# Kernel tuning notes

Measured on AMD Instinct MI355X. Metric: run time of the kernel, lower is better.

The kernel has to match this reference:

```python
import jax, jax.numpy as jnp
import numpy as np

N = 50000          # nodes
E = 800000         # edges (before self-loops)
F_IN = 128         # num_features
HEADS = 4
OUT = 128 // HEADS # per-head channels = num_hidden // heads
NEG_SLOPE = 0.2    # PyG GATConv default


def setup_inputs() -> dict:
    key = jax.random.key(0)
    ks = jax.random.split(key, 10)
    x = jax.random.normal(ks[0], (N, F_IN), jnp.float32)
    edge_index = jax.random.randint(ks[1], (2, E), 0, N, dtype=jnp.int64)
    sW = 1.0 / np.sqrt(F_IN)
    sA = 1.0 / np.sqrt(OUT)
    return {
        "x": x,
        "edge_index": edge_index,
        "W1": jax.random.normal(ks[2], (F_IN, HEADS * OUT), jnp.float32) * sW,
        "a_src1": jax.random.normal(ks[3], (HEADS, OUT), jnp.float32) * sA,
        "a_dst1": jax.random.normal(ks[4], (HEADS, OUT), jnp.float32) * sA,
        "b1": jnp.zeros((HEADS * OUT,), jnp.float32),
        "W2": jax.random.normal(ks[5], (HEADS * OUT, HEADS * OUT), jnp.float32) * sW,
        "a_src2": jax.random.normal(ks[6], (HEADS, OUT), jnp.float32) * sA,
        "a_dst2": jax.random.normal(ks[7], (HEADS, OUT), jnp.float32) * sA,
        "b2": jnp.zeros((HEADS * OUT,), jnp.float32),
    }


def gat_conv(x, src, dst, W, a_src, a_dst, b):
    """One GATConv layer (PyG semantics, concat heads, self-loops already in src/dst)."""
    n = x.shape[0]
    h = (x @ W).reshape(n, HEADS, OUT)                 # [N, H, C]
    # per-node attention halves, gathered per edge -> [Etot, H]
    alpha = (h * a_src).sum(-1)[src] + (h * a_dst).sum(-1)[dst]
    alpha = jax.nn.leaky_relu(alpha, NEG_SLOPE)
    # softmax over incoming edges of each destination node (stable)
    amax = jax.ops.segment_max(alpha, dst, num_segments=n)
    ex = jnp.exp(alpha - amax[dst])
    denom = jax.ops.segment_sum(ex, dst, num_segments=n)
    attn = ex / (denom[dst] + 1e-16)                    # [Etot, H]
    # weighted message scatter-add
    out = jax.ops.segment_sum(h[src] * attn[..., None], dst, num_segments=n)
    return out.reshape(n, HEADS * OUT) + b


def reference(x, edge_index, W1, a_src1, a_dst1, b1, W2, a_src2, a_dst2, b2):
    loops = jnp.arange(N, dtype=edge_index.dtype)       # PyG add_self_loops=True
    src = jnp.concatenate([edge_index[0], loops])
    dst = jnp.concatenate([edge_index[1], loops])
    h = jax.nn.relu(gat_conv(x, src, dst, W1, a_src1, a_dst1, b1))
    # dropout = identity in eval mode
    h = jax.nn.relu(gat_conv(h, src, dst, W2, a_src2, a_dst2, b2))
    return h
```

## Files before the change

### kernel.cpp

```cpp
#include <hip/hip_runtime.h>
#include <hip/hip_fp16.h>
#include <cstdint>
#include <cstddef>

#define NN 50000
#define EE 800000
#define ETOT (EE + NN)
#define FD 128
#define NH 4
#define NEG_SLOPE 0.2f

#define BSHIFT 10
#define BSIZE 1024
#define NBKT ((NN + BSIZE - 1) / BSIZE)
#define CAPG 20000
#define CHUNK 2048
#define P1_BLOCKS ((ETOT + CHUNK - 1) / CHUNK)

typedef _Float16 half8 __attribute__((ext_vector_type(8)));
typedef float f32x4 __attribute__((ext_vector_type(4)));


__global__ __launch_bounds__(256) void bin_kernel(const int* __restrict__ ei,
                                                  int* __restrict__ gcnt,
                                                  uint32_t* __restrict__ gbkt) {
    __shared__ int lcnt[NBKT];
    __shared__ int gb[NBKT];
    const int t = threadIdx.x;
    if (t < NBKT) lcnt[t] = 0;
    __syncthreads();
    const int base = blockIdx.x * CHUNK;
    uint32_t pk[8]; int bk[8]; int sl[8];
    #pragma unroll
    for (int j = 0; j < 8; ++j) {
        int e = base + j * 256 + t;
        bk[j] = -1;
        if (e < ETOT) {
            int src, dst;
            if (e < EE) { src = ei[e]; dst = ei[EE + e]; }
            else        { src = e - EE; dst = src; }
            int b = dst >> BSHIFT;
            bk[j] = b;
            pk[j] = (uint32_t)src | ((uint32_t)(dst & (BSIZE - 1)) << 16);
            sl[j] = atomicAdd(&lcnt[b], 1);
        }
    }
    __syncthreads();
    if (t < NBKT) gb[t] = atomicAdd(&gcnt[t], lcnt[t]);
    __syncthreads();
    #pragma unroll
    for (int j = 0; j < 8; ++j)
        if (bk[j] >= 0)
            gbkt[(size_t)bk[j] * CAPG + gb[bk[j]] + sl[j]] = pk[j];
}

__global__ void bktscan_kernel(const int* __restrict__ gcnt, int* __restrict__ bbase,
                               int* __restrict__ row_ptr) {
    int lane = threadIdx.x;
    int v = (lane < NBKT) ? gcnt[lane] : 0;
    int inc = v;
    #pragma unroll
    for (int off = 1; off < 64; off <<= 1) {
        int u = __shfl_up(inc, off);
        if (lane >= off) inc += u;
    }
    if (lane < NBKT) bbase[lane] = inc - v;
    if (lane == 0) row_ptr[NN] = ETOT;
}

__global__ __launch_bounds__(1024) void sort_kernel(const int* __restrict__ gcnt,
                                                    const int* __restrict__ bbase,
                                                    const uint32_t* __restrict__ gbkt,
                                                    int* __restrict__ row_ptr,
                                                    int* __restrict__ csr) {
    __shared__ int cnt[BSIZE];
    __shared__ int pfx[BSIZE];
    __shared__ int wsum[16];
    const int b = blockIdx.x;
    const int t = threadIdx.x;
    const int count = gcnt[b];
    const int cbase = bbase[b];
    const int dstBase = b << BSHIFT;
    const int ndst = (NN - dstBase < BSIZE) ? (NN - dstBase) : BSIZE;
    const uint32_t* mybkt = gbkt + (size_t)b * CAPG;
    cnt[t] = 0;
    __syncthreads();
    for (int i = t; i < count; i += 1024)
        atomicAdd(&cnt[mybkt[i] >> 16], 1);
    __syncthreads();
    int v = cnt[t];
    int inc = v;
    const int lane = t & 63, wid = t >> 6;
    #pragma unroll
    for (int off = 1; off < 64; off <<= 1) {
        int u = __shfl_up(inc, off);
        if (lane >= off) inc += u;
    }
    if (lane == 63) wsum[wid] = inc;
    __syncthreads();
    if (t < 16) {
        int w = wsum[t]; int wi = w;
        #pragma unroll
        for (int off = 1; off < 16; off <<= 1) {
            int u = __shfl_up(wi, off);
            if (t >= off) wi += u;
        }
        wsum[t] = wi - w;
    }
    __syncthreads();
    int excl = wsum[wid] + inc - v;
    pfx[t] = excl;
    if (t < ndst) row_ptr[dstBase + t] = cbase + excl;
    cnt[t] = 0;
    __syncthreads();
    for (int i = t; i < count; i += 1024) {
        uint32_t pkv = mybkt[i];
        int dl = pkv >> 16;
        int r = atomicAdd(&cnt[dl], 1);
        csr[cbase + pfx[dl] + r] = (int)(pkv & 0xFFFFu);
    }
}


__global__ void prep_kernel(const float* __restrict__ W1, const float* __restrict__ W2,
                            uint4* __restrict__ Wf1, uint4* __restrict__ Wf2) {
    const float* W = blockIdx.x ? W2 : W1;
    uint4* Wf = blockIdx.x ? Wf2 : Wf1;
    for (int s = threadIdx.x; s < 2048; s += 256) {
        int fi = s >> 6;
        int lane = s & 63;
        int ct = fi >> 2, ks = fi & 3;
        int col = ct * 16 + (lane & 15);
        int kb = ks * 32 + (lane >> 4) * 8;
        half8 h;
        #pragma unroll
        for (int j = 0; j < 8; ++j) h[j] = (_Float16)W[(kb + j) * FD + col];
        Wf[s] = *(uint4*)&h;
    }
}


__global__ __launch_bounds__(256) void gemm_kernel(const float* __restrict__ X,
                                                   const uint4* __restrict__ Wf,
                                                   __half* __restrict__ Hh) {
    const int tid = threadIdx.x;
    const int wv = tid >> 6, lane = tid & 63;
    const int l15 = lane & 15, lg = lane >> 4;
    const int rowA = blockIdx.x * 64 + wv * 16 + l15;
    const int rA = (rowA < NN) ? rowA : NN - 1;
    half8 a[4];
    #pragma unroll
    for (int ks = 0; ks < 4; ++ks) {
        int kb = ks * 32 + lg * 8;
        float4 x0 = *(const float4*)&X[(size_t)rA * FD + kb];
        float4 x1 = *(const float4*)&X[(size_t)rA * FD + kb + 4];
        a[ks][0] = (_Float16)x0.x; a[ks][1] = (_Float16)x0.y;
        a[ks][2] = (_Float16)x0.z; a[ks][3] = (_Float16)x0.w;
        a[ks][4] = (_Float16)x1.x; a[ks][5] = (_Float16)x1.y;
        a[ks][6] = (_Float16)x1.z; a[ks][7] = (_Float16)x1.w;
    }
    const int rowC = blockIdx.x * 64 + wv * 16 + lg * 4;
    #pragma unroll
    for (int ct = 0; ct < 8; ++ct) {
        uint4 braw[4];
        #pragma unroll
        for (int ks = 0; ks < 4; ++ks) braw[ks] = Wf[(ct * 4 + ks) * 64 + lane];
        f32x4 acc = {0.f, 0.f, 0.f, 0.f};
        #pragma unroll
        for (int ks = 0; ks < 4; ++ks) {
            half8 b = *(half8*)&braw[ks];
            acc = __builtin_amdgcn_mfma_f32_16x16x32_f16(a[ks], b, acc, 0, 0, 0);
        }
        #pragma unroll
        for (int r = 0; r < 4; ++r) {
            int gr = rowC + r;
            if (gr < NN) Hh[(size_t)gr * FD + ct * 16 + l15] = __float2half(acc[r]);
        }
    }
}


__global__ __launch_bounds__(256) void adot_kernel(const __half* __restrict__ H,
                                                   const float* __restrict__ a_src,
                                                   const float* __restrict__ a_dst,
                                                   float* __restrict__ AS,
                                                   float* __restrict__ AD) {
    int gt = blockIdx.x * 256 + threadIdx.x;
    int n = gt >> 4;
    int l = gt & 15;
    if (n >= NN) return;
    union { uint4 u; __half2 q[4]; } hv;
    hv.u = *(const uint4*)&H[(size_t)n * FD + l * 8];
    float ps = 0.f, pd = 0.f;
    #pragma unroll
    for (int j = 0; j < 4; ++j) {
        float2 f = __half22float2(hv.q[j]);
        ps += f.x * a_src[l * 8 + 2 * j] + f.y * a_src[l * 8 + 2 * j + 1];
        pd += f.x * a_dst[l * 8 + 2 * j] + f.y * a_dst[l * 8 + 2 * j + 1];
    }
    ps += __shfl_xor(ps, 1); ps += __shfl_xor(ps, 2);
    pd += __shfl_xor(pd, 1); pd += __shfl_xor(pd, 2);
    if ((l & 3) == 0) {
        AS[n * NH + (l >> 2)] = ps;
        AD[n * NH + (l >> 2)] = pd;
    }
}


__device__ __forceinline__ float sel4(float a0, float a1, float a2, float a3, int h) {
    float lo = (h & 1) ? a1 : a0;
    float hi = (h & 1) ? a3 : a2;
    return (h & 2) ? hi : lo;
}

__global__ __launch_bounds__(256) void agg_kernel(const __half* __restrict__ H,
                                                  const float* __restrict__ AS,
                                                  const float* __restrict__ AD,
                                                  const int* __restrict__ row_ptr,
                                                  const int* __restrict__ csr_src,
                                                  const float* __restrict__ bias,
                                                  float* __restrict__ Out) {
    __shared__ float sP[8][32][5];
    __shared__ int   sS[8][32];
    const int wave = threadIdx.x >> 6;
    const int lane = threadIdx.x & 63;
    const int sub  = lane >> 5;
    const int sl   = lane & 31;
    const int ws   = wave * 2 + sub;
    const int n = blockIdx.x * 8 + ws;
    const int start = row_ptr[n], end = row_ptr[n + 1];
    const int h0 = sl >> 3;
    const float4 adv = *(const float4*)&AD[n * NH];
    float s[NH] = {0.f, 0.f, 0.f, 0.f};
    float acc0 = 0.f, acc1 = 0.f, acc2 = 0.f, acc3 = 0.f;

    for (int base = start; base < end; base += 32) {
        int cn = end - base; if (cn > 32) cn = 32;
        int my_src = 0;
        float al[NH];
        if (sl < cn) {
            my_src = csr_src[base + sl];
            float4 asv = *(const float4*)&AS[my_src * NH];
            al[0] = asv.x + adv.x; al[1] = asv.y + adv.y;
            al[2] = asv.z + adv.z; al[3] = asv.w + adv.w;
        }
        sS[ws][sl] = my_src;
        #pragma unroll
        for (int h = 0; h < NH; ++h) {
            float a = al[h];
            a = (a > 0.f) ? a : NEG_SLOPE * a;
            float p = (sl < cn) ? __expf(a) : 0.f;
            sP[ws][sl][h] = p;
            #pragma unroll
            for (int off = 16; off; off >>= 1) p += __shfl_xor(p, off, 32);
            s[h] += p;
        }
        #pragma unroll 4
        for (int e = 0; e < cn; ++e) {
            float pm = sP[ws][e][h0];
            int se = sS[ws][e];
            union { uint2 u; __half2 q[2]; } hv;
            hv.u = *(const uint2*)&H[(size_t)se * FD + sl * 4];
            float2 f0 = __half22float2(hv.q[0]);
            float2 f1 = __half22float2(hv.q[1]);
            acc0 += pm * f0.x; acc1 += pm * f0.y;
            acc2 += pm * f1.x; acc3 += pm * f1.y;
        }
    }
    float sh = sel4(s[0], s[1], s[2], s[3], h0);
    float inv = 1.f / (sh + 1e-16f);
    const float4 bv = *(const float4*)&bias[sl * 4];
    float4 ov;
    ov.x = fmaxf(acc0 * inv + bv.x, 0.f);
    ov.y = fmaxf(acc1 * inv + bv.y, 0.f);
    ov.z = fmaxf(acc2 * inv + bv.z, 0.f);
    ov.w = fmaxf(acc3 * inv + bv.w, 0.f);
    *(float4*)&Out[(size_t)n * FD + sl * 4] = ov;
}


extern "C" void kernel_launch(void* const* d_in, const int* in_sizes, int n_in,
                              void* d_out, int out_size, void* d_ws, size_t ws_size,
                              hipStream_t stream) {
    const float* x     = (const float*)d_in[0];
    const int*   ei    = (const int*)d_in[1];
    const float* W1    = (const float*)d_in[2];
    const float* asrc1 = (const float*)d_in[3];
    const float* adst1 = (const float*)d_in[4];
    const float* b1    = (const float*)d_in[5];
    const float* W2    = (const float*)d_in[6];
    const float* asrc2 = (const float*)d_in[7];
    const float* adst2 = (const float*)d_in[8];
    const float* b2    = (const float*)d_in[9];
    float* out = (float*)d_out;

    char* p = (char*)d_ws;
    auto alloc = [&](size_t bytes) {
        char* q = p;
        p += (bytes + 255) & ~(size_t)255;
        return q;
    };
    int*      row_ptr = (int*)alloc((NN + 1) * sizeof(int));
    int*      gcnt    = (int*)alloc(NBKT * sizeof(int));
    int*      bbase   = (int*)alloc(NBKT * sizeof(int));
    uint32_t* gbkt    = (uint32_t*)alloc((size_t)NBKT * CAPG * sizeof(uint32_t));
    int*      csr     = (int*)alloc((size_t)ETOT * sizeof(int));
    float*    AS      = (float*)alloc((size_t)NN * NH * sizeof(float));
    float*    AD      = (float*)alloc((size_t)NN * NH * sizeof(float));
    __half*   Hh      = (__half*)alloc((size_t)NN * FD * sizeof(__half));
    uint4*    Wf1     = (uint4*)alloc(2048 * sizeof(uint4));
    uint4*    Wf2     = (uint4*)alloc(2048 * sizeof(uint4));
    (void)ws_size; (void)in_sizes; (void)n_in; (void)out_size;

    hipMemsetAsync(gcnt, 0, NBKT * sizeof(int), stream);
    bin_kernel<<<P1_BLOCKS, 256, 0, stream>>>(ei, gcnt, gbkt);
    prep_kernel<<<2, 256, 0, stream>>>(W1, W2, Wf1, Wf2);
    bktscan_kernel<<<1, 64, 0, stream>>>(gcnt, bbase, row_ptr);
    sort_kernel<<<NBKT, 1024, 0, stream>>>(gcnt, bbase, gbkt, row_ptr, csr);

    gemm_kernel<<<(NN + 63) / 64, 256, 0, stream>>>(x, Wf1, Hh);
    adot_kernel<<<(NN * 16 + 255) / 256, 256, 0, stream>>>(Hh, asrc1, adst1, AS, AD);
    agg_kernel<<<NN / 8, 256, 0, stream>>>(Hh, AS, AD, row_ptr, csr, b1, out);

    gemm_kernel<<<(NN + 63) / 64, 256, 0, stream>>>(out, Wf2, Hh);
    adot_kernel<<<(NN * 16 + 255) / 256, 256, 0, stream>>>(Hh, asrc2, adst2, AS, AD);
    agg_kernel<<<NN / 8, 256, 0, stream>>>(Hh, AS, AD, row_ptr, csr, b2, out);
}
```

Before: 157.4 us.

## Fuse attention dot products into GEMM epilogue and merge preprocessing launches

The per-node attention projections (AS/AD) are now computed inside the GEMM epilogue from the fp32 MFMA accumulators, using a butterfly shuffle transpose-reduce. This removes the separate adot kernel and its re-read of H. The weight-prep work is folded into extra blocks of the binning kernel, and the bucket scan is recomputed redundantly inside each sort block. The memset becomes a tiny kernel, so two fewer launches run per layer pipeline. In exchange the GEMM epilogue uses more registers and shuffles, and the attention logits now come from fp32 accumulators instead of fp16-rounded H, which slightly changes numerics.

After: 193.4 us. 1.23x slower.

```diff
diff --git a/kernel.cpp b/kernel.cpp
--- a/kernel.cpp
+++ b/kernel.cpp
@@ -21,9 +21,35 @@
 typedef float f32x4 __attribute__((ext_vector_type(4)));
 
 
+__global__ void zero_kernel(int* __restrict__ gcnt) {
+    int t = threadIdx.x;
+    if (t < NBKT) gcnt[t] = 0;
+}
+
+
 __global__ __launch_bounds__(256) void bin_kernel(const int* __restrict__ ei,
                                                   int* __restrict__ gcnt,
-                                                  uint32_t* __restrict__ gbkt) {
+                                                  uint32_t* __restrict__ gbkt,
+                                                  const float* __restrict__ W1,
+                                                  const float* __restrict__ W2,
+                                                  uint4* __restrict__ Wf1,
+                                                  uint4* __restrict__ Wf2) {
+    if (blockIdx.x >= P1_BLOCKS) {
+        const float* W = (blockIdx.x - P1_BLOCKS) ? W2 : W1;
+        uint4* Wf = (blockIdx.x - P1_BLOCKS) ? Wf2 : Wf1;
+        for (int s = threadIdx.x; s < 2048; s += 256) {
+            int fi = s >> 6;
+            int lane = s & 63;
+            int ct = fi >> 2, ks = fi & 3;
+            int col = ct * 16 + (lane & 15);
+            int kb = ks * 32 + (lane >> 4) * 8;
+            half8 h;
+            #pragma unroll
+            for (int j = 0; j < 8; ++j) h[j] = (_Float16)W[(kb + j) * FD + col];
+            Wf[s] = *(uint4*)&h;
+        }
+        return;
+    }
     __shared__ int lcnt[NBKT];
     __shared__ int gb[NBKT];
     const int t = threadIdx.x;
@@ -54,37 +80,34 @@
             gbkt[(size_t)bk[j] * CAPG + gb[bk[j]] + sl[j]] = pk[j];
 }
 
-__global__ void bktscan_kernel(const int* __restrict__ gcnt, int* __restrict__ bbase,
-                               int* __restrict__ row_ptr) {
-    int lane = threadIdx.x;
-    int v = (lane < NBKT) ? gcnt[lane] : 0;
-    int inc = v;
-    #pragma unroll
-    for (int off = 1; off < 64; off <<= 1) {
-        int u = __shfl_up(inc, off);
-        if (lane >= off) inc += u;
-    }
-    if (lane < NBKT) bbase[lane] = inc - v;
-    if (lane == 0) row_ptr[NN] = ETOT;
-}
 
 __global__ __launch_bounds__(1024) void sort_kernel(const int* __restrict__ gcnt,
-                                                    const int* __restrict__ bbase,
                                                     const uint32_t* __restrict__ gbkt,
                                                     int* __restrict__ row_ptr,
                                                     int* __restrict__ csr) {
     __shared__ int cnt[BSIZE];
     __shared__ int pfx[BSIZE];
     __shared__ int wsum[16];
+    __shared__ int sCbase;
     const int b = blockIdx.x;
     const int t = threadIdx.x;
     const int count = gcnt[b];
-    const int cbase = bbase[b];
     const int dstBase = b << BSHIFT;
     const int ndst = (NN - dstBase < BSIZE) ? (NN - dstBase) : BSIZE;
     const uint32_t* mybkt = gbkt + (size_t)b * CAPG;
     cnt[t] = 0;
-    __syncthreads();
+    if (t < 64) {
+        int v = (t < NBKT) ? gcnt[t] : 0;
+        int inc = v;
+        #pragma unroll
+        for (int off = 1; off < 64; off <<= 1) {
+            int u = __shfl_up(inc, off);
+            if (t >= off) inc += u;
+        }
+        if (t == b) sCbase = inc - v;
+    }
+    __syncthreads();
+    const int cbase = sCbase;
     for (int i = t; i < count; i += 1024)
         atomicAdd(&cnt[mybkt[i] >> 16], 1);
     __syncthreads();
@@ -111,6 +134,7 @@
     int excl = wsum[wid] + inc - v;
     pfx[t] = excl;
     if (t < ndst) row_ptr[dstBase + t] = cbase + excl;
+    if (b == NBKT - 1 && t == 0) row_ptr[NN] = ETOT;
     cnt[t] = 0;
     __syncthreads();
     for (int i = t; i < count; i += 1024) {
@@ -122,27 +146,13 @@
 }
 
 
-__global__ void prep_kernel(const float* __restrict__ W1, const float* __restrict__ W2,
-                            uint4* __restrict__ Wf1, uint4* __restrict__ Wf2) {
-    const float* W = blockIdx.x ? W2 : W1;
-    uint4* Wf = blockIdx.x ? Wf2 : Wf1;
-    for (int s = threadIdx.x; s < 2048; s += 256) {
-        int fi = s >> 6;
-        int lane = s & 63;
-        int ct = fi >> 2, ks = fi & 3;
-        int col = ct * 16 + (lane & 15);
-        int kb = ks * 32 + (lane >> 4) * 8;
-        half8 h;
-        #pragma unroll
-        for (int j = 0; j < 8; ++j) h[j] = (_Float16)W[(kb + j) * FD + col];
-        Wf[s] = *(uint4*)&h;
-    }
-}
-
-
 __global__ __launch_bounds__(256) void gemm_kernel(const float* __restrict__ X,
                                                    const uint4* __restrict__ Wf,
-                                                   __half* __restrict__ Hh) {
+                                                   const float* __restrict__ a_src,
+                                                   const float* __restrict__ a_dst,
+                                                   __half* __restrict__ Hh,
+                                                   float* __restrict__ AS,
+                                                   float* __restrict__ AD) {
     const int tid = threadIdx.x;
     const int wv = tid >> 6, lane = tid & 63;
     const int l15 = lane & 15, lg = lane >> 4;
@@ -159,7 +169,14 @@
         a[ks][4] = (_Float16)x1.x; a[ks][5] = (_Float16)x1.y;
         a[ks][6] = (_Float16)x1.z; a[ks][7] = (_Float16)x1.w;
     }
+    float asr[8], adr[8];
+    #pragma unroll
+    for (int ct = 0; ct < 8; ++ct) {
+        asr[ct] = a_src[ct * 16 + l15];
+        adr[ct] = a_dst[ct * 16 + l15];
+    }
     const int rowC = blockIdx.x * 64 + wv * 16 + lg * 4;
+    float ps[NH][4] = {}, pd[NH][4] = {};
     #pragma unroll
     for (int ct = 0; ct < 8; ++ct) {
         uint4 braw[4];
@@ -168,8 +185,13 @@
         f32x4 acc = {0.f, 0.f, 0.f, 0.f};
         #pragma unroll
         for (int ks = 0; ks < 4; ++ks) {
-            half8 b = *(half8*)&braw[ks];
-            acc = __builtin_amdgcn_mfma_f32_16x16x32_f16(a[ks], b, acc, 0, 0, 0);
+            half8 bfr = *(half8*)&braw[ks];
+            acc = __builtin_amdgcn_mfma_f32_16x16x32_f16(a[ks], bfr, acc, 0, 0, 0);
+        }
+        #pragma unroll
+        for (int r = 0; r < 4; ++r) {
+            ps[ct >> 1][r] += acc[r] * asr[ct];
+            pd[ct >> 1][r] += acc[r] * adr[ct];
         }
         #pragma unroll
         for (int r = 0; r < 4; ++r) {
@@ -177,32 +199,33 @@
             if (gr < NN) Hh[(size_t)gr * FD + ct * 16 + l15] = __float2half(acc[r]);
         }
     }
-}
-
-
-__global__ __launch_bounds__(256) void adot_kernel(const __half* __restrict__ H,
-                                                   const float* __restrict__ a_src,
-                                                   const float* __restrict__ a_dst,
-                                                   float* __restrict__ AS,
-                                                   float* __restrict__ AD) {
-    int gt = blockIdx.x * 256 + threadIdx.x;
-    int n = gt >> 4;
-    int l = gt & 15;
-    if (n >= NN) return;
-    union { uint4 u; __half2 q[4]; } hv;
-    hv.u = *(const uint4*)&H[(size_t)n * FD + l * 8];
-    float ps = 0.f, pd = 0.f;
-    #pragma unroll
-    for (int j = 0; j < 4; ++j) {
-        float2 f = __half22float2(hv.q[j]);
-        ps += f.x * a_src[l * 8 + 2 * j] + f.y * a_src[l * 8 + 2 * j + 1];
-        pd += f.x * a_dst[l * 8 + 2 * j] + f.y * a_dst[l * 8 + 2 * j + 1];
-    }
-    ps += __shfl_xor(ps, 1); ps += __shfl_xor(ps, 2);
-    pd += __shfl_xor(pd, 1); pd += __shfl_xor(pd, 2);
-    if ((l & 3) == 0) {
-        AS[n * NH + (l >> 2)] = ps;
-        AD[n * NH + (l >> 2)] = pd;
+    float V[32];
+    #pragma unroll
+    for (int h = 0; h < NH; ++h)
+        #pragma unroll
+        for (int r = 0; r < 4; ++r) {
+            V[(h << 2) | r] = ps[h][r];
+            V[16 + ((h << 2) | r)] = pd[h][r];
+        }
+    #pragma unroll
+    for (int m = 8; m >= 1; m >>= 1) {
+        const int n = m * 4;
+        const bool up = (l15 & m) != 0;
+        #pragma unroll
+        for (int i = 0; i < 16; ++i) {
+            if (i >= n / 2) break;
+            float send = up ? V[i] : V[i + n / 2];
+            float recv = __shfl_xor(send, m);
+            V[i] = (up ? V[i + n / 2] : V[i]) + recv;
+        }
+    }
+    {
+        int h = (((l15 >> 2) & 1) << 1) | ((l15 >> 1) & 1);
+        int rb = (l15 & 1) * 2;
+        float* T = (l15 & 8) ? AD : AS;
+        int gr0 = rowC + rb;
+        if (gr0 < NN)     T[gr0 * NH + h]       = V[0];
+        if (gr0 + 1 < NN) T[(gr0 + 1) * NH + h] = V[1];
     }
 }
 
@@ -247,13 +270,13 @@
         sS[ws][sl] = my_src;
         #pragma unroll
         for (int h = 0; h < NH; ++h) {
-            float a = al[h];
-            a = (a > 0.f) ? a : NEG_SLOPE * a;
-            float p = (sl < cn) ? __expf(a) : 0.f;
-            sP[ws][sl][h] = p;
+            float aa = al[h];
+            aa = (aa > 0.f) ? aa : NEG_SLOPE * aa;
+            float pp = (sl < cn) ? __expf(aa) : 0.f;
+            sP[ws][sl][h] = pp;
             #pragma unroll
-            for (int off = 16; off; off >>= 1) p += __shfl_xor(p, off, 32);
-            s[h] += p;
+            for (int off = 16; off; off >>= 1) pp += __shfl_xor(pp, off, 32);
+            s[h] += pp;
         }
         #pragma unroll 4
         for (int e = 0; e < cn; ++e) {
@@ -302,7 +325,6 @@
     };
     int*      row_ptr = (int*)alloc((NN + 1) * sizeof(int));
     int*      gcnt    = (int*)alloc(NBKT * sizeof(int));
-    int*      bbase   = (int*)alloc(NBKT * sizeof(int));
     uint32_t* gbkt    = (uint32_t*)alloc((size_t)NBKT * CAPG * sizeof(uint32_t));
     int*      csr     = (int*)alloc((size_t)ETOT * sizeof(int));
     float*    AS      = (float*)alloc((size_t)NN * NH * sizeof(float));
@@ -312,17 +334,13 @@
     uint4*    Wf2     = (uint4*)alloc(2048 * sizeof(uint4));
     (void)ws_size; (void)in_sizes; (void)n_in; (void)out_size;
 
-    hipMemsetAsync(gcnt, 0, NBKT * sizeof(int), stream);
-    bin_kernel<<<P1_BLOCKS, 256, 0, stream>>>(ei, gcnt, gbkt);
-    prep_kernel<<<2, 256, 0, stream>>>(W1, W2, Wf1, Wf2);
-    bktscan_kernel<<<1, 64, 0, stream>>>(gcnt, bbase, row_ptr);
-    sort_kernel<<<NBKT, 1024, 0, stream>>>(gcnt, bbase, gbkt, row_ptr, csr);
-
-    gemm_kernel<<<(NN + 63) / 64, 256, 0, stream>>>(x, Wf1, Hh);
-    adot_kernel<<<(NN * 16 + 255) / 256, 256, 0, stream>>>(Hh, asrc1, adst1, AS, AD);
+    zero_kernel<<<1, 64, 0, stream>>>(gcnt);
+    bin_kernel<<<P1_BLOCKS + 2, 256, 0, stream>>>(ei, gcnt, gbkt, W1, W2, Wf1, Wf2);
+    sort_kernel<<<NBKT, 1024, 0, stream>>>(gcnt, gbkt, row_ptr, csr);
+
+    gemm_kernel<<<(NN + 63) / 64, 256, 0, stream>>>(x, Wf1, asrc1, adst1, Hh, AS, AD);
     agg_kernel<<<NN / 8, 256, 0, stream>>>(Hh, AS, AD, row_ptr, csr, b1, out);
 
-    gemm_kernel<<<(NN + 63) / 64, 256, 0, stream>>>(out, Wf2, Hh);
-    adot_kernel<<<(NN * 16 + 255) / 256, 256, 0, stream>>>(Hh, asrc2, adst2, AS, AD);
+    gemm_kernel<<<(NN + 63) / 64, 256, 0, stream>>>(out, Wf2, asrc2, adst2, Hh, AS, AD);
     agg_kernel<<<NN / 8, 256, 0, stream>>>(Hh, AS, AD, row_ptr, csr, b2, out);
 }
```
